# Performance work log

Hardware: AMD Instinct MI355X
Metric: run time of the kernel (lower is better)

Reference implementation:

```python
import jax, jax.numpy as jnp
import numpy as np

N, D, F, E, TOP_K = 8192, 1024, 2048, 8, 2


def setup_inputs() -> dict:
    key = jax.random.key(0)
    ks = jax.random.split(key, 8)
    s = 0.02
    x = jax.random.normal(ks[0], (N, D), dtype=jnp.float32)
    Wr = jax.random.normal(ks[1], (D, E), dtype=jnp.float32) * s  # router
    br = jnp.zeros((E,), jnp.float32)
    W1 = jax.random.normal(ks[2], (E, D, F), dtype=jnp.float32) * s  # expert FFN in
    b1 = jnp.zeros((E, F), jnp.float32)
    W2 = jax.random.normal(ks[3], (E, F, D), dtype=jnp.float32) * s  # expert FFN out
    b2 = jnp.zeros((E, D), jnp. float32)
    return {"x": x, "Wr": Wr, "br": br, "W1": W1, "b1": b1, "W2": W2, "b2": b2}


def reference(x, Wr, br, W1, b1, W2, b2):
    # Router: per-token expert logits -> softmax probabilities -> top-k sampler.
    logits = x @ Wr + br                         # [N, E]
    probs = jax.nn.softmax(logits, axis=-1)      # [N, E]
    top_p, top_i = jax.lax.top_k(probs, TOP_K)   # [N, K]
    # Combine weights: prob mass only on the selected top-k experts per token.
    w = (jax.nn.one_hot(top_i, E, dtype=x.dtype) * top_p[..., None]).sum(axis=1)  # [N, E]
    # Per-expert gather-compute-scatter, expressed as masked full-batch expert FFN
    # (identical math: tokens not routed to expert e have weight 0).
    out = jnp.zeros((x.shape[0], W2.shape[-1]), dtype=x.dtype)
    for e in range(E):  # small fixed loop over structurally distinct experts
        h = jax.nn.gelu(x @ W1[e] + b1[e])       # [N, F]
        y = h @ W2[e] + b2[e]                    # [N, D]
        out = out + w[:, e:e + 1] * y            # weighted scatter-add combine
    return out
```

## Files before the change

kernel.cpp:

```cpp
#include <hip/hip_runtime.h>
#include <hip/hip_bf16.h>


#define N_TOK 8192
#define DIM   1024
#define FF    2048
#define NE    8

typedef unsigned short ushort_t;
typedef __bf16 bf16x8 __attribute__((ext_vector_type(8)));
typedef float  f32x4  __attribute__((ext_vector_type(4)));
typedef unsigned short u16x8 __attribute__((ext_vector_type(8)));

__device__ __forceinline__ ushort_t f2bf(float f) {
    union { float f; unsigned int u; } v; v.f = f;
    unsigned int r = (v.u + 0x7FFFu + ((v.u >> 16) & 1u)) >> 16;
    return (ushort_t)r;
}

__device__ __forceinline__ void gload_lds16(const ushort_t* g, ushort_t* l) {
    __builtin_amdgcn_global_load_lds(
        (const __attribute__((address_space(1))) void*)g,
        (__attribute__((address_space(3))) void*)l,
        16, 0, 0);
}

__global__ __launch_bounds__(256) void convert_x_kernel(
    const float* __restrict__ x, ushort_t* __restrict__ xb)
{
    size_t i = ((size_t)blockIdx.x * 256 + threadIdx.x) * 8;
    float4 a = *reinterpret_cast<const float4*>(x + i);
    float4 b = *reinterpret_cast<const float4*>(x + i + 4);
    u16x8 o;
    o[0] = f2bf(a.x); o[1] = f2bf(a.y); o[2] = f2bf(a.z); o[3] = f2bf(a.w);
    o[4] = f2bf(b.x); o[5] = f2bf(b.y); o[6] = f2bf(b.z); o[7] = f2bf(b.w);
    *reinterpret_cast<u16x8*>(xb + i) = o;
}

__global__ void transpose_conv_kernel(
    const float* __restrict__ in, ushort_t* __restrict__ out, int R, int C)
{
    __shared__ float tile[32][33];
    const int e = blockIdx.z;
    const float* I = in + (size_t)e * R * C;
    ushort_t*    O = out + (size_t)e * R * C;
    const int c0 = blockIdx.x * 32, r0 = blockIdx.y * 32;
    const int tx = threadIdx.x, ty = threadIdx.y;
#pragma unroll
    for (int j = 0; j < 32; j += 8)
        tile[ty + j][tx] = I[(size_t)(r0 + ty + j) * C + (c0 + tx)];
    __syncthreads();
#pragma unroll
    for (int j = 0; j < 32; j += 8)
        O[(size_t)(c0 + ty + j) * R + (r0 + tx)] = f2bf(tile[tx][ty + j]);
}

__global__ __launch_bounds__(256) void router_kernel(
    const float* __restrict__ x, const float* __restrict__ Wr, const float* __restrict__ br,
    int* __restrict__ cnt, int* __restrict__ tok_list, float* __restrict__ w_list)
{
    __shared__ int   se0[64], se1[64];
    __shared__ float sw0[64], sw1[64];

    const int wid  = threadIdx.x >> 6;
    const int lane = threadIdx.x & 63;
    const int tblk = blockIdx.x * 64;

    for (int i = 0; i < 16; ++i) {
        const int li = wid * 16 + i;
        const int t  = tblk + li;
        const float* xr = x + (size_t)t * DIM;

        float acc[NE];
#pragma unroll
        for (int e = 0; e < NE; ++e) acc[e] = 0.f;
        for (int d = lane; d < DIM; d += 64) {
            float xv = xr[d];
            const float4* w4 = reinterpret_cast<const float4*>(Wr + (size_t)d * NE);
            float4 w0 = w4[0], w1 = w4[1];
            acc[0] += xv * w0.x; acc[1] += xv * w0.y; acc[2] += xv * w0.z; acc[3] += xv * w0.w;
            acc[4] += xv * w1.x; acc[5] += xv * w1.y; acc[6] += xv * w1.z; acc[7] += xv * w1.w;
        }
#pragma unroll
        for (int e = 0; e < NE; ++e) {
            for (int off = 32; off > 0; off >>= 1)
                acc[e] += __shfl_down(acc[e], off, 64);
        }
        if (lane == 0) {
            float l[NE];
#pragma unroll
            for (int e = 0; e < NE; ++e) l[e] = acc[e] + br[e];
            float mx = l[0];
#pragma unroll
            for (int e = 1; e < NE; ++e) mx = fmaxf(mx, l[e]);
            float p[NE], s = 0.f;
#pragma unroll
            for (int e = 0; e < NE; ++e) { p[e] = expf(l[e] - mx); s += p[e]; }
            float inv = 1.f / s;
            int e0 = 0;
#pragma unroll
            for (int e = 1; e < NE; ++e) if (l[e] > l[e0]) e0 = e;
            int e1 = (e0 == 0) ? 1 : 0;
#pragma unroll
            for (int e = 0; e < NE; ++e) if (e != e0 && l[e] > l[e1]) e1 = e;
            se0[li] = e0; sw0[li] = p[e0] * inv;
            se1[li] = e1; sw1[li] = p[e1] * inv;
        }
    }
    __syncthreads();

    if (threadIdx.x < 64) {
        const int t  = tblk + lane;
        const int e0 = se0[lane], e1 = se1[lane];
        const unsigned long long below = ((unsigned long long)1 << lane) - 1;
        int p0 = 0, p1 = 0;
#pragma unroll
        for (int e = 0; e < NE; ++e) {
            unsigned long long m0 = __ballot(e0 == e);
            unsigned long long m1 = __ballot(e1 == e);
            int c = __popcll(m0) + __popcll(m1);
            int b = 0;
            if (lane == e && c) b = atomicAdd(&cnt[e], c);
            b = __shfl(b, e, 64);
            if (e0 == e) p0 = b + __popcll(m0 & below);
            if (e1 == e) p1 = b + __popcll(m0) + __popcll(m1 & below);
        }
        tok_list[e0 * N_TOK + p0] = t;  w_list[e0 * N_TOK + p0] = sw0[lane];
        tok_list[e1 * N_TOK + p1] = t;  w_list[e1 * N_TOK + p1] = sw1[lane];
    }
}

__global__ void scan_kernel(const int* __restrict__ cnt, int* __restrict__ offs)
{
    if (threadIdx.x == 0 && blockIdx.x == 0) {
        int s = 0;
        for (int e = 0; e < NE; ++e) { offs[e] = s; s += cnt[e]; }
        offs[NE] = s;
    }
}

template <int MODE>
__global__ __launch_bounds__(256) void moe_gemm_kernel(
    const ushort_t* __restrict__ A,
    const ushort_t* __restrict__ Bt,
    const float*    __restrict__ bias,
    const int*      __restrict__ cnt,
    const int*      __restrict__ offs,
    const int*      __restrict__ tok_list,
    const float*    __restrict__ w_list,
    ushort_t*       __restrict__ hout,
    float*          __restrict__ out,
    int K, int NCOL)
{
    const int e = blockIdx.z;
    const int cnt_e = cnt[e];

    int wg;
    if (MODE == 0) {
        const int cpx = gridDim.x >> 3;
        wg = (blockIdx.x & 7) * cpx + (blockIdx.x >> 3);
    } else {
        wg = blockIdx.x;
    }
    const int mb = wg & 63;
    const int nb = wg >> 6;

    const int m0 = mb * 128;
    if (m0 >= cnt_e) return;
    const int n0 = nb * 128;
    const int offs_e = offs[e];

    __shared__ ushort_t As[3][128 * 32];
    __shared__ ushort_t Bs[3][128 * 32];

    const int tid = threadIdx.x;

    size_t asrc[2], bsrc[2];
#pragma unroll
    for (int j = 0; j < 2; ++j) {
        int c = tid + 256 * j;
        int row   = c >> 2;
        int chunk = (c & 3) ^ ((row >> 1) & 3);
        int entry = m0 + row;
        size_t arow;
        if (MODE == 0) {
            int tok = (entry < cnt_e) ? tok_list[e * N_TOK + entry] : 0;
            arow = (size_t)tok * K;
        } else {
            arow = (size_t)(offs_e + entry) * K;
        }
        asrc[j] = arow + (size_t)chunk * 8;
        int col = n0 + row;
        bsrc[j] = ((size_t)e * NCOL + col) * K + (size_t)chunk * 8;
    }

    f32x4 acc[4][4];
#pragma unroll
    for (int m = 0; m < 4; ++m)
#pragma unroll
        for (int n = 0; n < 4; ++n)
            acc[m][n] = (f32x4){0.f, 0.f, 0.f, 0.f};

    const int lane = tid & 63;
    const int wid  = tid >> 6;
    const int wr = (wid >> 1) * 64;
    const int wc = (wid & 1) * 64;
    const int la = lane & 15;
    const int kc = lane >> 4;

    auto STAGE = [&](int t, int b) {
        int k0 = t * 32;
#pragma unroll
        for (int j = 0; j < 2; ++j) {
            gload_lds16(A  + asrc[j] + k0, &As[b][(tid + 256 * j) * 8]);
            gload_lds16(Bt + bsrc[j] + k0, &Bs[b][(tid + 256 * j) * 8]);
        }
    };

    auto COMPUTE = [&](int b) {
        bf16x8 af[4], bfr[4];
#pragma unroll
        for (int m = 0; m < 4; ++m) {
            int r = wr + m * 16 + la;
            af[m] = *reinterpret_cast<const bf16x8*>(&As[b][(r * 4 + (kc ^ ((r >> 1) & 3))) * 8]);
        }
#pragma unroll
        for (int n = 0; n < 4; ++n) {
            int r = wc + n * 16 + la;
            bfr[n] = *reinterpret_cast<const bf16x8*>(&Bs[b][(r * 4 + (kc ^ ((r >> 1) & 3))) * 8]);
        }
#pragma unroll
        for (int m = 0; m < 4; ++m)
#pragma unroll
            for (int n = 0; n < 4; ++n)
                acc[m][n] = __builtin_amdgcn_mfma_f32_16x16x32_bf16(af[m], bfr[n], acc[m][n], 0, 0, 0);
    };

    const int nk = K / 32;
    STAGE(0, 0);
    STAGE(1, 1);
    asm volatile("s_waitcnt vmcnt(4)" ::: "memory");
    __builtin_amdgcn_s_barrier();
    for (int t = 0; t < nk; ++t) {
        if (t + 2 < nk) STAGE(t + 2, (t + 2) % 3);
        COMPUTE(t % 3);
        if (t + 1 < nk) {
            if (t + 2 < nk) asm volatile("s_waitcnt vmcnt(4)" ::: "memory");
            else            asm volatile("s_waitcnt vmcnt(0)" ::: "memory");
            __builtin_amdgcn_s_barrier();
        }
    }

#pragma unroll
    for (int m = 0; m < 4; ++m) {
        int rbase = wr + m * 16 + (lane >> 4) * 4;
#pragma unroll
        for (int n = 0; n < 4; ++n) {
            int gcol = n0 + wc + n * 16 + la;
            float bi = bias[(size_t)e * NCOL + gcol];
#pragma unroll
            for (int jj = 0; jj < 4; ++jj) {
                int entry = m0 + rbase + jj;
                if (entry < cnt_e) {
                    float v = acc[m][n][jj] + bi;
                    if (MODE == 0) {
                        float u = 0.7978845608028654f * (v + 0.044715f * v * v * v);
                        float g = 0.5f * v * (1.f + tanhf(u));
                        hout[(size_t)(offs_e + entry) * NCOL + gcol] = f2bf(g);
                    } else {
                        int tok  = tok_list[e * N_TOK + entry];
                        float w  = w_list  [e * N_TOK + entry];
                        atomicAdd(&out[(size_t)tok * NCOL + gcol], w * v);
                    }
                }
            }
        }
    }
}

extern "C" void kernel_launch(void* const* d_in, const int* in_sizes, int n_in,
                              void* d_out, int out_size, void* d_ws, size_t ws_size,
                              hipStream_t stream)
{
    const float* x  = (const float*)d_in[0];
    const float* Wr = (const float*)d_in[1];
    const float* br = (const float*)d_in[2];
    const float* W1 = (const float*)d_in[3];
    const float* b1 = (const float*)d_in[4];
    const float* W2 = (const float*)d_in[5];
    const float* b2 = (const float*)d_in[6];
    float* out = (float*)d_out;

    char* ws = (char*)d_ws;
    size_t off = 0;
    auto alloc = [&](size_t bytes) -> void* {
        void* p = ws + off;
        off = (off + bytes + 255) & ~(size_t)255;
        return p;
    };
    ushort_t* xb  = (ushort_t*)alloc((size_t)N_TOK * DIM * 2);
    ushort_t* w1t = (ushort_t*)alloc((size_t)NE * DIM * FF * 2);
    ushort_t* w2t = (ushort_t*)alloc((size_t)NE * DIM * FF * 2);
    ushort_t* h   = (ushort_t*)alloc(((size_t)2 * N_TOK + 128) * FF * 2);
    int*      cnt = (int*)alloc(NE * sizeof(int));
    int*      offs= (int*)alloc((NE + 1) * sizeof(int));
    int*   tok_list = (int*)alloc((size_t)NE * N_TOK * sizeof(int));
    float* w_list   = (float*)alloc((size_t)NE * N_TOK * sizeof(float));
    (void)ws_size; (void)in_sizes; (void)n_in;

    hipMemsetAsync(out, 0, (size_t)out_size * sizeof(float), stream);
    hipMemsetAsync(cnt, 0, NE * sizeof(int), stream);

    convert_x_kernel<<<(N_TOK * DIM) / (8 * 256), 256, 0, stream>>>(x, xb);
    transpose_conv_kernel<<<dim3(FF / 32, DIM / 32, NE), dim3(32, 8), 0, stream>>>(W1, w1t, DIM, FF);
    transpose_conv_kernel<<<dim3(DIM / 32, FF / 32, NE), dim3(32, 8), 0, stream>>>(W2, w2t, FF, DIM);
    router_kernel<<<N_TOK / 64, 256, 0, stream>>>(x, Wr, br, cnt, tok_list, w_list);
    scan_kernel<<<1, 64, 0, stream>>>(cnt, offs);

    moe_gemm_kernel<0><<<dim3(64 * (FF / 128), 1, NE), 256, 0, stream>>>(
        xb, w1t, b1, cnt, offs, tok_list, w_list, h, nullptr, DIM, FF);
    moe_gemm_kernel<1><<<dim3(64 * (DIM / 128), 1, NE), 256, 0, stream>>>(
        h, w2t, b2, cnt, offs, tok_list, w_list, nullptr, out, FF, DIM);
}
```

Measured before the change: 566.9 us.

## Pre-gather routed tokens into packed bf16 buffer; unify block swizzle and pipeline loop

Replaces the dense x-to-bf16 conversion with a gather kernel that writes each expert's routed tokens into a contiguous packed bf16 buffer, so the first expert GEMM reads contiguous rows instead of going through tok_list indirection. The GEMM2 launch now also uses the XCD-aware block swizzle, and the main K loop is restructured so the wait and barrier come before the stage and compute, with the last iteration peeled. The cost is an extra packed buffer write covering 2N rows in place of the N-row conversion.

```diff
diff --git a/kernel.cpp b/kernel.cpp
--- a/kernel.cpp
+++ b/kernel.cpp
@@ -23,18 +23,6 @@
         (const __attribute__((address_space(1))) void*)g,
         (__attribute__((address_space(3))) void*)l,
         16, 0, 0);
-}
-
-__global__ __launch_bounds__(256) void convert_x_kernel(
-    const float* __restrict__ x, ushort_t* __restrict__ xb)
-{
-    size_t i = ((size_t)blockIdx.x * 256 + threadIdx.x) * 8;
-    float4 a = *reinterpret_cast<const float4*>(x + i);
-    float4 b = *reinterpret_cast<const float4*>(x + i + 4);
-    u16x8 o;
-    o[0] = f2bf(a.x); o[1] = f2bf(a.y); o[2] = f2bf(a.z); o[3] = f2bf(a.w);
-    o[4] = f2bf(b.x); o[5] = f2bf(b.y); o[6] = f2bf(b.z); o[7] = f2bf(b.w);
-    *reinterpret_cast<u16x8*>(xb + i) = o;
 }
 
 __global__ void transpose_conv_kernel(
@@ -137,6 +125,26 @@
         for (int e = 0; e < NE; ++e) { offs[e] = s; s += cnt[e]; }
         offs[NE] = s;
     }
+}
+
+__global__ __launch_bounds__(256) void gather_a_kernel(
+    const float* __restrict__ x, const int* __restrict__ offs,
+    const int* __restrict__ tok_list, ushort_t* __restrict__ xpack)
+{
+    const int c   = blockIdx.x * 256 + threadIdx.x;
+    const int row = c >> 7;
+    int e = 0;
+#pragma unroll
+    for (int k = 1; k < NE; ++k) e += (row >= offs[k]);
+    const int tok = tok_list[e * N_TOK + (row - offs[e])];
+    const int d0  = (c & 127) << 3;
+    const float* src = x + ((size_t)tok << 10) + d0;
+    float4 a = *reinterpret_cast<const float4*>(src);
+    float4 b = *reinterpret_cast<const float4*>(src + 4);
+    u16x8 o;
+    o[0] = f2bf(a.x); o[1] = f2bf(a.y); o[2] = f2bf(a.z); o[3] = f2bf(a.w);
+    o[4] = f2bf(b.x); o[5] = f2bf(b.y); o[6] = f2bf(b.z); o[7] = f2bf(b.w);
+    *reinterpret_cast<u16x8*>(xpack + ((size_t)row << 10) + d0) = o;
 }
 
 template <int MODE>
@@ -155,15 +163,10 @@
     const int e = blockIdx.z;
     const int cnt_e = cnt[e];
 
-    int wg;
-    if (MODE == 0) {
-        const int cpx = gridDim.x >> 3;
-        wg = (blockIdx.x & 7) * cpx + (blockIdx.x >> 3);
-    } else {
-        wg = blockIdx.x;
-    }
-    const int mb = wg & 63;
-    const int nb = wg >> 6;
+    const int cpx = gridDim.x >> 3;
+    const int wg  = (blockIdx.x & 7) * cpx + (blockIdx.x >> 3);
+    const int mb  = wg & 63;
+    const int nb  = wg >> 6;
 
     const int m0 = mb * 128;
     if (m0 >= cnt_e) return;
@@ -184,8 +187,7 @@
         int entry = m0 + row;
         size_t arow;
         if (MODE == 0) {
-            int tok = (entry < cnt_e) ? tok_list[e * N_TOK + entry] : 0;
-            arow = (size_t)tok * K;
+            arow = (entry < cnt_e) ? (size_t)(offs_e + entry) * K : 0;
         } else {
             arow = (size_t)(offs_e + entry) * K;
         }
@@ -239,17 +241,15 @@
     const int nk = K / 32;
     STAGE(0, 0);
     STAGE(1, 1);
-    asm volatile("s_waitcnt vmcnt(4)" ::: "memory");
-    __builtin_amdgcn_s_barrier();
-    for (int t = 0; t < nk; ++t) {
+    for (int t = 0; t < nk - 1; ++t) {
+        asm volatile("s_waitcnt vmcnt(4)" ::: "memory");
+        __builtin_amdgcn_s_barrier();
         if (t + 2 < nk) STAGE(t + 2, (t + 2) % 3);
         COMPUTE(t % 3);
-        if (t + 1 < nk) {
-            if (t + 2 < nk) asm volatile("s_waitcnt vmcnt(4)" ::: "memory");
-            else            asm volatile("s_waitcnt vmcnt(0)" ::: "memory");
-            __builtin_amdgcn_s_barrier();
-        }
-    }
+    }
+    asm volatile("s_waitcnt vmcnt(0)" ::: "memory");
+    __builtin_amdgcn_s_barrier();
+    COMPUTE((nk - 1) % 3);
 
 #pragma unroll
     for (int m = 0; m < 4; ++m) {
@@ -298,9 +298,9 @@
         off = (off + bytes + 255) & ~(size_t)255;
         return p;
     };
-    ushort_t* xb  = (ushort_t*)alloc((size_t)N_TOK * DIM * 2);
     ushort_t* w1t = (ushort_t*)alloc((size_t)NE * DIM * FF * 2);
     ushort_t* w2t = (ushort_t*)alloc((size_t)NE * DIM * FF * 2);
+    ushort_t* xpack = (ushort_t*)alloc((size_t)2 * N_TOK * DIM * 2);
     ushort_t* h   = (ushort_t*)alloc(((size_t)2 * N_TOK + 128) * FF * 2);
     int*      cnt = (int*)alloc(NE * sizeof(int));
     int*      offs= (int*)alloc((NE + 1) * sizeof(int));
@@ -311,14 +311,14 @@
     hipMemsetAsync(out, 0, (size_t)out_size * sizeof(float), stream);
     hipMemsetAsync(cnt, 0, NE * sizeof(int), stream);
 
-    convert_x_kernel<<<(N_TOK * DIM) / (8 * 256), 256, 0, stream>>>(x, xb);
     transpose_conv_kernel<<<dim3(FF / 32, DIM / 32, NE), dim3(32, 8), 0, stream>>>(W1, w1t, DIM, FF);
     transpose_conv_kernel<<<dim3(DIM / 32, FF / 32, NE), dim3(32, 8), 0, stream>>>(W2, w2t, FF, DIM);
     router_kernel<<<N_TOK / 64, 256, 0, stream>>>(x, Wr, br, cnt, tok_list, w_list);
     scan_kernel<<<1, 64, 0, stream>>>(cnt, offs);
+    gather_a_kernel<<<(2 * N_TOK * DIM) / (8 * 256), 256, 0, stream>>>(x, offs, tok_list, xpack);
 
     moe_gemm_kernel<0><<<dim3(64 * (FF / 128), 1, NE), 256, 0, stream>>>(
-        xb, w1t, b1, cnt, offs, tok_list, w_list, h, nullptr, DIM, FF);
+        xpack, w1t, b1, cnt, offs, tok_list, w_list, h, nullptr, DIM, FF);
     moe_gemm_kernel<1><<<dim3(64 * (DIM / 128), 1, NE), 256, 0, stream>>>(
         h, w2t, b2, cnt, offs, tok_list, w_list, nullptr, out, FF, DIM);
 }
```

Measured after the change: 527.4 us. 1.08x faster.
